# Performance work log

Measured on AMD Instinct MI355X. Metric: run time of the kernel, lower is better.

The kernel has to match this reference:

```python
import jax, jax.numpy as jnp
import numpy as np

NUM_LAYERS = 4
NUM_HEADS = 8
D_MODEL = 256
D_FF = 1024
UNC_THRESHOLD = 0.3
B, L = 2, 2048


def _layer_norm(x, g, b, eps=1e-5):
    m = jnp.mean(x, axis=-1, keepdims=True)
    v = jnp.mean((x - m) ** 2, axis=-1, keepdims=True)
    return (x - m) * jax.lax.rsqrt(v + eps) * g + b


def setup_inputs() -> dict:
    key = jax.random.key(0)
    ks = jax.random.split(key, 32)
    D, F, Ly = D_MODEL, D_FF, NUM_LAYERS
    w = lambda k, shape: jax.random.normal(k, shape, dtype=jnp.float32) * 0.02
    return {
        'x': jax.random.normal(ks[0], (B, L, D), dtype=jnp.float32),
        'Win': w(ks[1], (D, D)), 'bin_': jnp.zeros((D,), jnp.float32),
        'Wq': w(ks[2], (Ly, D, D)), 'bq': jnp.zeros((Ly, D), jnp.float32),
        'Wk': w(ks[3], (Ly, D, D)), 'bk': jnp.zeros((Ly, D), jnp.float32),
        'Wv': w(ks[4], (Ly, D, D)), 'bv': jnp.zeros((Ly, D), jnp.float32),
        'Wo': w(ks[5], (Ly, D, D)), 'bo': jnp.zeros((Ly, D), jnp.float32),
        'ev_scale': jnp.ones((Ly,), jnp.float32),
        'ev_bias': jnp.zeros((Ly,), jnp.float32),
        'W1': w(ks[6], (Ly, D, F)), 'b1': jnp.zeros((Ly, F), jnp.float32),
        'W2': w(ks[7], (Ly, F, D)), 'b2': jnp.zeros((Ly, D), jnp.float32),
        'n1g': jnp.ones((Ly, D), jnp.float32), 'n1b': jnp.zeros((Ly, D), jnp.float32),
        'n2g': jnp.ones((Ly, D), jnp.float32), 'n2b': jnp.zeros((Ly, D), jnp.float32),
        'fng': jnp.ones((D,), jnp.float32), 'fnb': jnp.zeros((D,), jnp.float32),
        'Wout': w(ks[8], (D, D)), 'bout': jnp.zeros((D,), jnp.float32),
    }


def _evidence_attention(x, Wq, bq, Wk, bk, Wv, bv, Wo, bo, scale, bias):
    b, l, d = x.shape
    hd = d // NUM_HEADS
    def heads(t):
        return t.reshape(b, l, NUM_HEADS, hd).transpose(0, 2, 1, 3)  # [B,H,L,hd]
    Q = heads(x @ Wq + bq)
    K = heads(x @ Wk + bk)
    V = heads(x @ Wv + bv)
    scores = jnp.einsum('bhqd,bhkd->bhqk', Q, K) / np.sqrt(hd).astype(np.float32)
    evidence = jnp.exp(scores) * scale + 1.0 + bias           # [B,H,L,L]
    denom = jnp.sum(evidence, axis=-1, keepdims=True)         # [B,H,L,1]
    uncertainty = (jnp.float32(l) / denom)[..., 0]            # [B,H,L]
    probs = evidence / denom
    attn = jnp.einsum('bhqk,bhkd->bhqd', probs, V)
    attn = attn.transpose(0, 2, 1, 3).reshape(b, l, d)
    return attn @ Wo + bo, uncertainty


def reference(x, Win, bin_, Wq, bq, Wk, bk, Wv, bv, Wo, bo, ev_scale, ev_bias,
              W1, b1, W2, b2, n1g, n1b, n2g, n2b, fng, fnb, Wout, bout):
    h = x @ Win + bin_
    total_unc = 0.0
    for i in range(NUM_LAYERS):
        attn_out, unc = _evidence_attention(
            _layer_norm(h, n1g[i], n1b[i]),
            Wq[i], bq[i], Wk[i], bk[i], Wv[i], bv[i], Wo[i], bo[i],
            ev_scale[i], ev_bias[i])
        h = h + attn_out
        ff = jax.nn.gelu(_layer_norm(h, n2g[i], n2b[i]) @ W1[i] + b1[i], approximate=False) @ W2[i] + b2[i]
        h = h + ff
        total_unc = total_unc + unc
    avg_unc = total_unc / NUM_LAYERS                          # [B,H,L]
    out = _layer_norm(h, fng, fnb) @ Wout + bout              # [B,L,D]
    should_abstain = avg_unc > UNC_THRESHOLD
    return out, avg_unc, should_abstain
```

## Files before the change

### kernel.cpp

```cpp
#include <hip/hip_runtime.h>
#include <hip/hip_bf16.h>
#include <math.h>

#define B_  2
#define L_  2048
#define D_  256
#define H_  8
#define HD_ 32
#define F_  1024
#define LY_ 4
#define M_  (B_*L_)

typedef __attribute__((ext_vector_type(8))) short bf16x8;
typedef __attribute__((ext_vector_type(4))) float f32x4;

static __device__ __forceinline__ short f2bf(float f) {
    return __builtin_bit_cast(short, __float2bfloat16(f));
}

static __device__ __forceinline__ void gload_lds16(const ushort* g, ushort* l) {
    __builtin_amdgcn_global_load_lds(
        (const __attribute__((address_space(1))) void*)g,
        (__attribute__((address_space(3))) void*)l, 16, 0, 0);
}

__global__ __launch_bounds__(256) void transpose_weights(
    const float* __restrict__ Win, const float* __restrict__ Wq,
    const float* __restrict__ Wk,  const float* __restrict__ Wv,
    const float* __restrict__ Wo,  const float* __restrict__ W1,
    const float* __restrict__ W2,  const float* __restrict__ Wout,
    ushort* __restrict__ T)
{
    const int bid = blockIdx.x;
    const float* src; ushort* dst; int K, N, tt;
    if (bid < 64)        { src = Win; dst = T; K = 256; N = 256; tt = bid; }
    else if (bid < 1088) {
        int i = bid - 64; int which = i >> 8; int l = (i >> 6) & 3; tt = i & 63;
        K = 256; N = 256;
        const float* s4[4] = {Wq, Wk, Wv, Wo};
        src = s4[which] + l * 65536;
        dst = T + 65536 * (1 + which * 4 + l);
    } else if (bid < 2112) {
        int i = bid - 1088; int l = i >> 8; tt = i & 255; K = 256; N = 1024;
        src = W1 + l * 262144; dst = T + 65536 * 17 + l * 262144;
    } else if (bid < 3136) {
        int i = bid - 2112; int l = i >> 8; tt = i & 255; K = 1024; N = 256;
        src = W2 + l * 262144; dst = T + 65536 * 17 + 1048576 + l * 262144;
    } else {
        src = Wout; dst = T + 65536 * 17 + 2097152; K = 256; N = 256; tt = bid - 3136;
    }
    const int ntn = N >> 5;
    const int tk = tt / ntn, tn = tt % ntn;
    __shared__ float ld[32][33];
    const int t = threadIdx.x;
    const int r = t >> 3, c4 = (t & 7) * 4;
    float4 v = *reinterpret_cast<const float4*>(&src[(size_t)(tk * 32 + r) * N + tn * 32 + c4]);
    ld[r][c4 + 0] = v.x; ld[r][c4 + 1] = v.y; ld[r][c4 + 2] = v.z; ld[r][c4 + 3] = v.w;
    __syncthreads();
    short4 o;
    o.x = f2bf(ld[c4 + 0][r]);
    o.y = f2bf(ld[c4 + 1][r]);
    o.z = f2bf(ld[c4 + 2][r]);
    o.w = f2bf(ld[c4 + 3][r]);
    *reinterpret_cast<short4*>(&dst[(size_t)(tn * 32 + r) * K + tk * 32 + c4]) = o;
}

template<int LNM>
__device__ __forceinline__ void core_f(
    const float* __restrict__ Hin, const float* __restrict__ lng,
    const float* __restrict__ lnb, const ushort* __restrict__ Wt,
    int row0, int col0, ushort* sLN, ushort* sW, f32x4 acc[2][2])
{
    const int tid  = threadIdx.x;
    const int lane = tid & 63;
    const int wid  = tid >> 6;
    const int wr = wid >> 1, wc = wid & 1;
    const int g = lane >> 4, nn = lane & 15;

    const int r0 = tid >> 3;
    const int sx = ((tid & 7) ^ (r0 & 7)) << 3;
    const ushort* Wp = &Wt[(size_t)(col0 + r0) * 256 + sx];
    ushort* ldsW = sW + wid * 512;
    gload_lds16(Wp,            ldsW);
    gload_lds16(Wp + 32 * 256, ldsW + 2048);

    const float4* hp = reinterpret_cast<const float4*>(Hin + (size_t)row0 * D_);
    float4 av[16];
#pragma unroll
    for (int j = 0; j < 16; ++j) av[j] = hp[j * 256 + tid];

    float4 g4, b4;
    if (LNM) {
        g4 = reinterpret_cast<const float4*>(lng)[lane];
        b4 = reinterpret_cast<const float4*>(lnb)[lane];
    }
#pragma unroll
    for (int j = 0; j < 16; ++j) {
        const float4 v = av[j];
        short4 o;
        if (LNM) {
            float s  = v.x + v.y + v.z + v.w;
            float s2 = v.x * v.x + v.y * v.y + v.z * v.z + v.w * v.w;
            s  += __shfl_xor(s, 1);  s  += __shfl_xor(s, 2);  s  += __shfl_xor(s, 4);
            s  += __shfl_xor(s, 8);  s  += __shfl_xor(s, 16); s  += __shfl_xor(s, 32);
            s2 += __shfl_xor(s2, 1); s2 += __shfl_xor(s2, 2); s2 += __shfl_xor(s2, 4);
            s2 += __shfl_xor(s2, 8); s2 += __shfl_xor(s2, 16); s2 += __shfl_xor(s2, 32);
            const float mean = s * (1.0f / D_);
            const float var  = s2 * (1.0f / D_) - mean * mean;
            const float rstd = rsqrtf(var + 1e-5f);
            o.x = f2bf((v.x - mean) * rstd * g4.x + b4.x);
            o.y = f2bf((v.y - mean) * rstd * g4.y + b4.y);
            o.z = f2bf((v.z - mean) * rstd * g4.z + b4.z);
            o.w = f2bf((v.w - mean) * rstd * g4.w + b4.w);
        } else {
            o.x = f2bf(v.x); o.y = f2bf(v.y); o.z = f2bf(v.z); o.w = f2bf(v.w);
        }
        *reinterpret_cast<short4*>(&sLN[(j * 4 + wid) * 264 + lane * 4]) = o;
    }
    __syncthreads();

    const int ra = (wr * 32 + nn) * 264, rb = ra + 16 * 264;
    const int rc = (wc * 32 + nn) * 64,  rd = rc + 16 * 64;
    const int m7 = nn & 7;

    int cur = 0;
#pragma unroll
    for (int k0 = 0; k0 < 256; k0 += 64) {
        if (k0 + 64 < 256) {
            ushort* lW = ldsW + (cur ^ 1) * 4096;
            gload_lds16(Wp + k0 + 64,            lW);
            gload_lds16(Wp + k0 + 64 + 32 * 256, lW + 2048);
        }
        const ushort* w = sW + cur * 4096;
#pragma unroll
        for (int sk = 0; sk < 2; ++sk) {
            const int ac = k0 + sk * 32 + g * 8;
            bf16x8 a0 = *reinterpret_cast<const bf16x8*>(&sLN[ra + ac]);
            bf16x8 a1 = *reinterpret_cast<const bf16x8*>(&sLN[rb + ac]);
            const int sw = ((sk * 4 + g) ^ m7) << 3;
            bf16x8 w0 = *reinterpret_cast<const bf16x8*>(&w[rc + sw]);
            bf16x8 w1 = *reinterpret_cast<const bf16x8*>(&w[rd + sw]);
            acc[0][0] = __builtin_amdgcn_mfma_f32_16x16x32_bf16(a0, w0, acc[0][0], 0, 0, 0);
            acc[0][1] = __builtin_amdgcn_mfma_f32_16x16x32_bf16(a0, w1, acc[0][1], 0, 0, 0);
            acc[1][0] = __builtin_amdgcn_mfma_f32_16x16x32_bf16(a1, w0, acc[1][0], 0, 0, 0);
            acc[1][1] = __builtin_amdgcn_mfma_f32_16x16x32_bf16(a1, w1, acc[1][1], 0, 0, 0);
        }
        __syncthreads();
        cur ^= 1;
    }
}

template<int LNM, int EPI, int OUTBF>
__global__ __launch_bounds__(256) void gemm_fused(
    const float* __restrict__ Hin, const float* __restrict__ lng,
    const float* __restrict__ lnb, const ushort* __restrict__ Wt,
    const float* __restrict__ bias, void* __restrict__ Cout, int N)
{
    __shared__ __align__(16) ushort sLN[64 * 264];
    __shared__ __align__(16) ushort sW[2 * 4096];
    const int row0 = blockIdx.y * 64, col0 = blockIdx.x * 64;
    f32x4 acc[2][2] = {};
    core_f<LNM>(Hin, lng, lnb, Wt, row0, col0, sLN, sW, acc);

    const int lane = threadIdx.x & 63;
    const int wid  = threadIdx.x >> 6;
    const int wr = wid >> 1, wc = wid & 1;
    const int g = lane >> 4, nn = lane & 15;
#pragma unroll
    for (int mi = 0; mi < 2; ++mi)
#pragma unroll
    for (int ni = 0; ni < 2; ++ni)
#pragma unroll
    for (int r = 0; r < 4; ++r) {
        const int m = row0 + wr * 32 + mi * 16 + g * 4 + r;
        const int c = col0 + wc * 32 + ni * 16 + nn;
        float v = acc[mi][ni][r] + bias[c];
        if (EPI == 1) v = 0.5f * v * (1.0f + erff(v * 0.70710678118654752f));
        if (OUTBF) ((ushort*)Cout)[(size_t)m * N + c] = (ushort)f2bf(v);
        else       ((float*)Cout)[(size_t)m * N + c] = v;
    }
}

__global__ __launch_bounds__(256) void gemm_qkv_f(
    const float* __restrict__ Hin, const float* __restrict__ lng,
    const float* __restrict__ lnb,
    const ushort* __restrict__ WqT, const ushort* __restrict__ WkT,
    const ushort* __restrict__ WvT,
    const float* __restrict__ bq, const float* __restrict__ bk,
    const float* __restrict__ bv,
    ushort* __restrict__ Qb, ushort* __restrict__ Kb, ushort* __restrict__ Vt)
{
    __shared__ __align__(16) ushort sLN[64 * 264];
    __shared__ __align__(16) ushort sW[2 * 4096];
    const int nb = blockIdx.x;
    const int wsel = nb >> 2;
    const int col0 = (nb & 3) * 64;
    const int row0 = blockIdx.y * 64;
    const ushort* Wt = (wsel == 0) ? WqT : (wsel == 1) ? WkT : WvT;
    const float* bias = (wsel == 0) ? bq : (wsel == 1) ? bk : bv;

    f32x4 acc[2][2] = {};
    core_f<1>(Hin, lng, lnb, Wt, row0, col0, sLN, sW, acc);

    const int lane = threadIdx.x & 63;
    const int wid  = threadIdx.x >> 6;
    const int wr = wid >> 1, wc = wid & 1;
    const int g = lane >> 4, nn = lane & 15;
    ushort* QK = (wsel == 0) ? Qb : Kb;
#pragma unroll
    for (int mi = 0; mi < 2; ++mi)
#pragma unroll
    for (int ni = 0; ni < 2; ++ni)
#pragma unroll
    for (int r = 0; r < 4; ++r) {
        const int m = row0 + wr * 32 + mi * 16 + g * 4 + r;
        const int c = col0 + wc * 32 + ni * 16 + nn;
        const float v = acc[mi][ni][r] + bias[c];
        if (wsel < 2) {
            QK[(size_t)m * D_ + c] = (ushort)f2bf(v);
        } else {
            const int b = m >> 11, l = m & 2047;
            const int h = c >> 5,  d = c & 31;
            Vt[(size_t)((b * 8 + h) * 32 + d) * L_ + l] = (ushort)f2bf(v);
        }
    }
}

__device__ __forceinline__ void gemm_core64(
    const ushort* __restrict__ A, const ushort* __restrict__ Wt, int K,
    int row0, int col0, ushort* sA, ushort* sW, f32x4 acc[2][2])
{
    const int tid  = threadIdx.x;
    const int lane = tid & 63;
    const int wid  = tid >> 6;
    const int wr = wid >> 1, wc = wid & 1;
    const int g = lane >> 4, nn = lane & 15;

    const int r0 = tid >> 3;
    const int sx = ((tid & 7) ^ (r0 & 7)) << 3;

    const ushort* Ap = &A[(size_t)(row0 + r0) * K + sx];
    const ushort* Wp = &Wt[(size_t)(col0 + r0) * K + sx];
    const size_t rstep = (size_t)32 * K;

    ushort* ldsA = sA + wid * 512;
    ushort* ldsW = sW + wid * 512;

    gload_lds16(Ap,         ldsA);
    gload_lds16(Ap + rstep, ldsA + 2048);
    gload_lds16(Wp,         ldsW);
    gload_lds16(Wp + rstep, ldsW + 2048);

    const int ra = (wr * 32 + nn) * 64, rb = ra + 16 * 64;
    const int rc = (wc * 32 + nn) * 64, rd = rc + 16 * 64;
    const int m7 = nn & 7;

    int cur = 0;
    __syncthreads();
    for (int k0 = 0; k0 < K; k0 += 64) {
        if (k0 + 64 < K) {
            ushort* lA = ldsA + (cur ^ 1) * 4096;
            ushort* lW = ldsW + (cur ^ 1) * 4096;
            gload_lds16(Ap + k0 + 64,         lA);
            gload_lds16(Ap + k0 + 64 + rstep, lA + 2048);
            gload_lds16(Wp + k0 + 64,         lW);
            gload_lds16(Wp + k0 + 64 + rstep, lW + 2048);
        }
        const ushort* a = sA + cur * 4096;
        const ushort* w = sW + cur * 4096;
#pragma unroll
        for (int sk = 0; sk < 2; ++sk) {
            const int sw = ((sk * 4 + g) ^ m7) << 3;
            bf16x8 a0 = *reinterpret_cast<const bf16x8*>(&a[ra + sw]);
            bf16x8 a1 = *reinterpret_cast<const bf16x8*>(&a[rb + sw]);
            bf16x8 w0 = *reinterpret_cast<const bf16x8*>(&w[rc + sw]);
            bf16x8 w1 = *reinterpret_cast<const bf16x8*>(&w[rd + sw]);
            acc[0][0] = __builtin_amdgcn_mfma_f32_16x16x32_bf16(a0, w0, acc[0][0], 0, 0, 0);
            acc[0][1] = __builtin_amdgcn_mfma_f32_16x16x32_bf16(a0, w1, acc[0][1], 0, 0, 0);
            acc[1][0] = __builtin_amdgcn_mfma_f32_16x16x32_bf16(a1, w0, acc[1][0], 0, 0, 0);
            acc[1][1] = __builtin_amdgcn_mfma_f32_16x16x32_bf16(a1, w1, acc[1][1], 0, 0, 0);
        }
        __syncthreads();
        cur ^= 1;
    }
}

__global__ __launch_bounds__(256) void gemm_res(
    const ushort* __restrict__ A, const ushort* __restrict__ Wt,
    const float* __restrict__ bias, float* __restrict__ C, int K)
{
    __shared__ __align__(16) ushort sA[2 * 4096];
    __shared__ __align__(16) ushort sW[2 * 4096];
    const int row0 = blockIdx.y * 64, col0 = blockIdx.x * 64;
    f32x4 acc[2][2] = {};
    gemm_core64(A, Wt, K, row0, col0, sA, sW, acc);

    const int lane = threadIdx.x & 63;
    const int wid  = threadIdx.x >> 6;
    const int wr = wid >> 1, wc = wid & 1;
    const int g = lane >> 4, nn = lane & 15;
#pragma unroll
    for (int mi = 0; mi < 2; ++mi)
#pragma unroll
    for (int ni = 0; ni < 2; ++ni)
#pragma unroll
    for (int r = 0; r < 4; ++r) {
        const int m = row0 + wr * 32 + mi * 16 + g * 4 + r;
        const int c = col0 + wc * 32 + ni * 16 + nn;
        C[(size_t)m * D_ + c] += acc[mi][ni][r] + bias[c];
    }
}

__global__ __launch_bounds__(256) void attn_mfma(
    const ushort* __restrict__ Qb, const ushort* __restrict__ Kb,
    const ushort* __restrict__ Vt, ushort* __restrict__ O,
    float* __restrict__ unc, const float* __restrict__ ev_scale,
    const float* __restrict__ ev_bias, int layer,
    float* __restrict__ out_unc, float* __restrict__ out_abst)
{
    const int bh = blockIdx.y;
    const int b  = bh >> 3;
    const int h  = bh & 7;
    const int tid  = threadIdx.x;
    const int wv   = tid >> 6;
    const int lane = tid & 63;
    const int g = lane >> 4;
    const int n = lane & 15;
    const int q  = blockIdx.x * 64 + wv * 16 + n;
    const float scale = ev_scale[layer];
    const float cb    = 1.0f + ev_bias[layer];
    const float isq   = 0.17677669529663687f;

    __shared__ __align__(16) ushort sK[2][64][40];
    __shared__ __align__(16) ushort sV[2][32][72];

    const size_t qk0 = (size_t)b * L_ * D_ + h * HD_;

    bf16x8 qf;
    {
        const bf16x8 qr = *reinterpret_cast<const bf16x8*>(&Qb[qk0 + (size_t)q * D_ + g * 8]);
#pragma unroll
        for (int j = 0; j < 8; ++j) {
            const float qv = __builtin_bit_cast(float, ((unsigned)(unsigned short)qr[j]) << 16);
            qf[j] = f2bf(qv * isq);
        }
    }
    bf16x8 ones;
#pragma unroll
    for (int j = 0; j < 8; ++j) ones[j] = (short)0x3F80;

    const int krow = tid >> 2, kch = (tid & 3) * 8;
    const int vrow = tid >> 3, vch = (tid & 7) * 8;
    const ushort* ksrc = Kb + qk0 + (size_t)krow * D_ + kch;
    const ushort* vsrc = Vt + (size_t)((b * 8 + h) * 32 + vrow) * L_ + vch;

    f32x4 acc0 = {0.f, 0.f, 0.f, 0.f};
    f32x4 acc1 = {0.f, 0.f, 0.f, 0.f};
    f32x4 accS = {0.f, 0.f, 0.f, 0.f};
    const f32x4 zero = {0.f, 0.f, 0.f, 0.f};

    bf16x8 kreg = *reinterpret_cast<const bf16x8*>(ksrc);
    bf16x8 vreg = *reinterpret_cast<const bf16x8*>(vsrc);

    int cur = 0;
    for (int t = 0; t < L_; t += 64) {
        *reinterpret_cast<bf16x8*>(&sK[cur][krow][kch]) = kreg;
        *reinterpret_cast<bf16x8*>(&sV[cur][vrow][vch]) = vreg;
        if (t + 64 < L_) {
            kreg = *reinterpret_cast<const bf16x8*>(ksrc + (size_t)(t + 64) * D_);
            vreg = *reinterpret_cast<const bf16x8*>(vsrc + (t + 64));
        }
        __syncthreads();

#pragma unroll
        for (int tt = 0; tt < 64; tt += 32) {
            bf16x8 kf0 = *reinterpret_cast<const bf16x8*>(&sK[cur][tt + n][g * 8]);
            bf16x8 kf1 = *reinterpret_cast<const bf16x8*>(&sK[cur][tt + 16 + n][g * 8]);

            f32x4 s0 = __builtin_amdgcn_mfma_f32_16x16x32_bf16(kf0, qf, zero, 0, 0, 0);
            f32x4 s1 = __builtin_amdgcn_mfma_f32_16x16x32_bf16(kf1, qf, zero, 0, 0, 0);

            short4 va = *reinterpret_cast<const short4*>(&sV[cur][n][tt + g * 4]);
            short4 vb = *reinterpret_cast<const short4*>(&sV[cur][n][tt + 16 + g * 4]);
            short4 vc = *reinterpret_cast<const short4*>(&sV[cur][n + 16][tt + g * 4]);
            short4 vd = *reinterpret_cast<const short4*>(&sV[cur][n + 16][tt + 16 + g * 4]);
            bf16x8 vf0 = {va.x, va.y, va.z, va.w, vb.x, vb.y, vb.z, vb.w};
            bf16x8 vf1 = {vc.x, vc.y, vc.z, vc.w, vd.x, vd.y, vd.z, vd.w};

            bf16x8 pa;
#pragma unroll
            for (int r = 0; r < 4; ++r) pa[r]     = f2bf(fmaf(__expf(s0[r]), scale, cb));
#pragma unroll
            for (int r = 0; r < 4; ++r) pa[r + 4] = f2bf(fmaf(__expf(s1[r]), scale, cb));

            acc0 = __builtin_amdgcn_mfma_f32_16x16x32_bf16(vf0, pa, acc0, 0, 0, 0);
            acc1 = __builtin_amdgcn_mfma_f32_16x16x32_bf16(vf1, pa, acc1, 0, 0, 0);
            accS = __builtin_amdgcn_mfma_f32_16x16x32_bf16(ones, pa, accS, 0, 0, 0);
        }
        cur ^= 1;
    }

    const float inv = 1.0f / accS[0];

    ushort* op = &O[qk0 + (size_t)q * D_ + g * 4];
    short4 o0 = {f2bf(acc0[0] * inv), f2bf(acc0[1] * inv), f2bf(acc0[2] * inv), f2bf(acc0[3] * inv)};
    short4 o1 = {f2bf(acc1[0] * inv), f2bf(acc1[1] * inv), f2bf(acc1[2] * inv), f2bf(acc1[3] * inv)};
    *reinterpret_cast<short4*>(op)      = o0;
    *reinterpret_cast<short4*>(op + 16) = o1;

    if (g == 0) {
        const float u = (float)L_ * inv;
        const int uidx = bh * L_ + q;
        if (layer == 0) {
            unc[uidx] = u;
        } else if (layer < LY_ - 1) {
            unc[uidx] += u;
        } else {
            const float avg = (unc[uidx] + u) * 0.25f;
            out_unc[uidx]  = avg;
            out_abst[uidx] = (avg > 0.3f) ? 1.0f : 0.0f;
        }
    }
}

extern "C" void kernel_launch(void* const* d_in, const int* in_sizes, int n_in,
                              void* d_out, int out_size, void* d_ws, size_t ws_size,
                              hipStream_t stream)
{
    const float* x    = (const float*)d_in[0];
    const float* Win  = (const float*)d_in[1];
    const float* bin_ = (const float*)d_in[2];
    const float* Wq   = (const float*)d_in[3];
    const float* bq   = (const float*)d_in[4];
    const float* Wk   = (const float*)d_in[5];
    const float* bk   = (const float*)d_in[6];
    const float* Wv   = (const float*)d_in[7];
    const float* bv   = (const float*)d_in[8];
    const float* Wo   = (const float*)d_in[9];
    const float* bo   = (const float*)d_in[10];
    const float* evs  = (const float*)d_in[11];
    const float* evb  = (const float*)d_in[12];
    const float* W1   = (const float*)d_in[13];
    const float* b1   = (const float*)d_in[14];
    const float* W2   = (const float*)d_in[15];
    const float* b2   = (const float*)d_in[16];
    const float* n1g  = (const float*)d_in[17];
    const float* n1b  = (const float*)d_in[18];
    const float* n2g  = (const float*)d_in[19];
    const float* n2b  = (const float*)d_in[20];
    const float* fng  = (const float*)d_in[21];
    const float* fnb  = (const float*)d_in[22];
    const float* Wout = (const float*)d_in[23];
    const float* bout = (const float*)d_in[24];

    char* ws = (char*)d_ws;
    float*  h    = (float*) (ws);
    ushort* Qb   = (ushort*)(ws + (6  << 20));
    ushort* Kb   = (ushort*)(ws + (8  << 20));
    ushort* Vt   = (ushort*)(ws + (10 << 20));
    ushort* Ob   = (ushort*)(ws + (12 << 20));
    ushort* ffb  = (ushort*)(ws + (4  << 20));
    float*  unc  = (float*) (ws + (14 << 20));
    ushort* T    = (ushort*)(ws + (15 << 20));

    ushort* winT  = T;
    ushort* woutT = T + 65536 * 17 + 2097152;

    float* out_main = (float*)d_out;
    float* out_unc  = out_main + M_ * D_;
    float* out_abst = out_unc + B_ * H_ * L_;

    const dim3 blk(256);
    const dim3 g256(4, 64);
    const dim3 g1024(16, 64);
    const dim3 gqkv(12, 64);
    const dim3 gattn(L_ / 64, B_ * H_);

    transpose_weights<<<3200, blk, 0, stream>>>(Win, Wq, Wk, Wv, Wo, W1, W2, Wout, T);
    gemm_fused<0, 0, 0><<<g256, blk, 0, stream>>>(x, nullptr, nullptr, winT, bin_, h, D_);

    for (int i = 0; i < LY_; ++i) {
        ushort* wqT = T + 65536 * (1 + i);
        ushort* wkT = T + 65536 * (5 + i);
        ushort* wvT = T + 65536 * (9 + i);
        ushort* woT = T + 65536 * (13 + i);
        ushort* w1T = T + 65536 * 17 + i * 262144;
        ushort* w2T = T + 65536 * 17 + 1048576 + i * 262144;

        gemm_qkv_f<<<gqkv, blk, 0, stream>>>(h, n1g + i * D_, n1b + i * D_,
                                             wqT, wkT, wvT,
                                             bq + i * D_, bk + i * D_, bv + i * D_,
                                             Qb, Kb, Vt);
        attn_mfma<<<gattn, blk, 0, stream>>>(Qb, Kb, Vt, Ob, unc, evs, evb, i,
                                             out_unc, out_abst);
        gemm_res<<<g256, blk, 0, stream>>>(Ob, woT, bo + i * D_, h, D_);
        gemm_fused<1, 1, 1><<<g1024, blk, 0, stream>>>(h, n2g + i * D_, n2b + i * D_,
                                                       w1T, b1 + i * F_, ffb, F_);
        gemm_res<<<g256, blk, 0, stream>>>(ffb, w2T, b2 + i * D_, h, F_);
    }

    gemm_fused<1, 0, 0><<<g256, blk, 0, stream>>>(h, fng, fnb, woutT, bout, out_main, D_);
}
```

Baseline: 323.2 us.

## Fuse out-proj, FFN and next-layer QKV into one row-block megakernel

Replaces the per-layer chain of separate GEMM launches (Wo residual, LN2+W1+GELU, W2 residual, LN1+QKV) with one kernel per layer. Each block handles 16 rows, keeps the residual and the FFN intermediate in LDS, and streams the full weight matrices through a double-buffered LDS tile. This removes the intermediate global round trips and several launches. In exchange, only 256 blocks run, each re-reads every weight matrix, and the large LDS footprint (about 120 KB) limits occupancy.

```diff
diff --git a/kernel.cpp b/kernel.cpp
--- a/kernel.cpp
+++ b/kernel.cpp
@@ -65,12 +65,13 @@
     *reinterpret_cast<short4*>(&dst[(size_t)(tn * 32 + r) * K + tk * 32 + c4]) = o;
 }
 
-template<int LNM>
-__device__ __forceinline__ void core_f(
-    const float* __restrict__ Hin, const float* __restrict__ lng,
-    const float* __restrict__ lnb, const ushort* __restrict__ Wt,
-    int row0, int col0, ushort* sLN, ushort* sW, f32x4 acc[2][2])
-{
+__global__ __launch_bounds__(256) void gemm_first(
+    const float* __restrict__ Hin, const ushort* __restrict__ Wt,
+    const float* __restrict__ bias, float* __restrict__ Cout)
+{
+    __shared__ __align__(16) ushort sLN[64 * 264];
+    __shared__ __align__(16) ushort sW[2 * 4096];
+    const int row0 = blockIdx.y * 64, col0 = blockIdx.x * 64;
     const int tid  = threadIdx.x;
     const int lane = tid & 63;
     const int wid  = tid >> 6;
@@ -85,36 +86,10 @@
     gload_lds16(Wp + 32 * 256, ldsW + 2048);
 
     const float4* hp = reinterpret_cast<const float4*>(Hin + (size_t)row0 * D_);
-    float4 av[16];
-#pragma unroll
-    for (int j = 0; j < 16; ++j) av[j] = hp[j * 256 + tid];
-
-    float4 g4, b4;
-    if (LNM) {
-        g4 = reinterpret_cast<const float4*>(lng)[lane];
-        b4 = reinterpret_cast<const float4*>(lnb)[lane];
-    }
 #pragma unroll
     for (int j = 0; j < 16; ++j) {
-        const float4 v = av[j];
-        short4 o;
-        if (LNM) {
-            float s  = v.x + v.y + v.z + v.w;
-            float s2 = v.x * v.x + v.y * v.y + v.z * v.z + v.w * v.w;
-            s  += __shfl_xor(s, 1);  s  += __shfl_xor(s, 2);  s  += __shfl_xor(s, 4);
-            s  += __shfl_xor(s, 8);  s  += __shfl_xor(s, 16); s  += __shfl_xor(s, 32);
-            s2 += __shfl_xor(s2, 1); s2 += __shfl_xor(s2, 2); s2 += __shfl_xor(s2, 4);
-            s2 += __shfl_xor(s2, 8); s2 += __shfl_xor(s2, 16); s2 += __shfl_xor(s2, 32);
-            const float mean = s * (1.0f / D_);
-            const float var  = s2 * (1.0f / D_) - mean * mean;
-            const float rstd = rsqrtf(var + 1e-5f);
-            o.x = f2bf((v.x - mean) * rstd * g4.x + b4.x);
-            o.y = f2bf((v.y - mean) * rstd * g4.y + b4.y);
-            o.z = f2bf((v.z - mean) * rstd * g4.z + b4.z);
-            o.w = f2bf((v.w - mean) * rstd * g4.w + b4.w);
-        } else {
-            o.x = f2bf(v.x); o.y = f2bf(v.y); o.z = f2bf(v.z); o.w = f2bf(v.w);
-        }
+        const float4 v = hp[j * 256 + tid];
+        short4 o = {f2bf(v.x), f2bf(v.y), f2bf(v.z), f2bf(v.w)};
         *reinterpret_cast<short4*>(&sLN[(j * 4 + wid) * 264 + lane * 4]) = o;
     }
     __syncthreads();
@@ -122,6 +97,7 @@
     const int ra = (wr * 32 + nn) * 264, rb = ra + 16 * 264;
     const int rc = (wc * 32 + nn) * 64,  rd = rc + 16 * 64;
     const int m7 = nn & 7;
+    f32x4 acc[2][2] = {};
 
     int cur = 0;
 #pragma unroll
@@ -148,24 +124,7 @@
         __syncthreads();
         cur ^= 1;
     }
-}
-
-template<int LNM, int EPI, int OUTBF>
-__global__ __launch_bounds__(256) void gemm_fused(
-    const float* __restrict__ Hin, const float* __restrict__ lng,
-    const float* __restrict__ lnb, const ushort* __restrict__ Wt,
-    const float* __restrict__ bias, void* __restrict__ Cout, int N)
-{
-    __shared__ __align__(16) ushort sLN[64 * 264];
-    __shared__ __align__(16) ushort sW[2 * 4096];
-    const int row0 = blockIdx.y * 64, col0 = blockIdx.x * 64;
-    f32x4 acc[2][2] = {};
-    core_f<LNM>(Hin, lng, lnb, Wt, row0, col0, sLN, sW, acc);
-
-    const int lane = threadIdx.x & 63;
-    const int wid  = threadIdx.x >> 6;
-    const int wr = wid >> 1, wc = wid & 1;
-    const int g = lane >> 4, nn = lane & 15;
+
 #pragma unroll
     for (int mi = 0; mi < 2; ++mi)
 #pragma unroll
@@ -174,140 +133,204 @@
     for (int r = 0; r < 4; ++r) {
         const int m = row0 + wr * 32 + mi * 16 + g * 4 + r;
         const int c = col0 + wc * 32 + ni * 16 + nn;
-        float v = acc[mi][ni][r] + bias[c];
-        if (EPI == 1) v = 0.5f * v * (1.0f + erff(v * 0.70710678118654752f));
-        if (OUTBF) ((ushort*)Cout)[(size_t)m * N + c] = (ushort)f2bf(v);
-        else       ((float*)Cout)[(size_t)m * N + c] = v;
-    }
-}
-
-__global__ __launch_bounds__(256) void gemm_qkv_f(
-    const float* __restrict__ Hin, const float* __restrict__ lng,
-    const float* __restrict__ lnb,
+        Cout[(size_t)m * D_ + c] = acc[mi][ni][r] + bias[c];
+    }
+}
+
+static __device__ __forceinline__ void stageW(
+    const ushort* __restrict__ W, int K, int k0, ushort* dst, int wid, int lane)
+{
+    const int rsub = lane >> 3;
+    const int slot = ((lane & 7) ^ (rsub & 7)) << 3;
+#pragma unroll
+    for (int q = 0; q < 8; ++q) {
+        const int r = (wid * 8 + q) * 8 + rsub;
+        gload_lds16(W + (size_t)r * K + k0 + slot, dst + (wid * 8 + q) * 512);
+    }
+}
+
+template<typename EPI>
+static __device__ __forceinline__ void gemm_nchunk(
+    const ushort* __restrict__ Wt, int K, const ushort* sA, int As,
+    ushort* sW, int wid, int lane, EPI epi)
+{
+    const int g = lane >> 4, nn = lane & 15;
+    stageW(Wt, K, 0, sW, wid, lane);
+    int cur = 0;
+    f32x4 acc[4] = {};
+    const int nkc = K >> 6;
+    for (int kc = 0; kc < nkc; ++kc) {
+        __syncthreads();
+        if (kc + 1 < nkc) stageW(Wt, K, (kc + 1) * 64, sW + (cur ^ 1) * 16384, wid, lane);
+        const ushort* w = sW + cur * 16384;
+#pragma unroll
+        for (int sk = 0; sk < 2; ++sk) {
+            bf16x8 a = *reinterpret_cast<const bf16x8*>(&sA[nn * As + kc * 64 + sk * 32 + g * 8]);
+            const int ws = ((sk * 4 + g) ^ (nn & 7)) << 3;
+#pragma unroll
+            for (int ni = 0; ni < 4; ++ni) {
+                const int wrow = wid * 64 + ni * 16 + nn;
+                bf16x8 wf = *reinterpret_cast<const bf16x8*>(&w[wrow * 64 + ws]);
+                acc[ni] = __builtin_amdgcn_mfma_f32_16x16x32_bf16(a, wf, acc[ni], 0, 0, 0);
+            }
+        }
+        cur ^= 1;
+    }
+    __syncthreads();
+    epi(acc);
+}
+
+static __device__ __forceinline__ void ln16(
+    const float* sH, ushort* sA, const float* __restrict__ gg,
+    const float* __restrict__ bb, int tid)
+{
+    const int row = tid >> 4, sc = (tid & 15) * 16;
+    float v[16];
+#pragma unroll
+    for (int j = 0; j < 16; ++j) v[j] = sH[row * 256 + sc + j];
+    float s = 0.f, s2 = 0.f;
+#pragma unroll
+    for (int j = 0; j < 16; ++j) { s += v[j]; s2 += v[j] * v[j]; }
+    s  += __shfl_xor(s, 1);  s  += __shfl_xor(s, 2);
+    s  += __shfl_xor(s, 4);  s  += __shfl_xor(s, 8);
+    s2 += __shfl_xor(s2, 1); s2 += __shfl_xor(s2, 2);
+    s2 += __shfl_xor(s2, 4); s2 += __shfl_xor(s2, 8);
+    const float mean = s * (1.0f / D_);
+    const float var  = s2 * (1.0f / D_) - mean * mean;
+    const float rstd = rsqrtf(var + 1e-5f);
+#pragma unroll
+    for (int j = 0; j < 16; ++j)
+        sA[row * 264 + sc + j] = (ushort)f2bf((v[j] - mean) * rstd * gg[sc + j] + bb[sc + j]);
+}
+
+template<int DO_FFN, int TAIL>
+__global__ __launch_bounds__(256) void mega(
+    const ushort* __restrict__ Ob, const ushort* __restrict__ WoT,
+    const float* __restrict__ bo, float* __restrict__ h,
+    const float* __restrict__ ln2g, const float* __restrict__ ln2b,
+    const ushort* __restrict__ W1T, const float* __restrict__ b1,
+    const ushort* __restrict__ W2T, const float* __restrict__ b2,
+    const float* __restrict__ ln1g, const float* __restrict__ ln1b,
     const ushort* __restrict__ WqT, const ushort* __restrict__ WkT,
     const ushort* __restrict__ WvT,
     const float* __restrict__ bq, const float* __restrict__ bk,
     const float* __restrict__ bv,
-    ushort* __restrict__ Qb, ushort* __restrict__ Kb, ushort* __restrict__ Vt)
-{
-    __shared__ __align__(16) ushort sLN[64 * 264];
-    __shared__ __align__(16) ushort sW[2 * 4096];
-    const int nb = blockIdx.x;
-    const int wsel = nb >> 2;
-    const int col0 = (nb & 3) * 64;
-    const int row0 = blockIdx.y * 64;
-    const ushort* Wt = (wsel == 0) ? WqT : (wsel == 1) ? WkT : WvT;
-    const float* bias = (wsel == 0) ? bq : (wsel == 1) ? bk : bv;
-
-    f32x4 acc[2][2] = {};
-    core_f<1>(Hin, lng, lnb, Wt, row0, col0, sLN, sW, acc);
-
-    const int lane = threadIdx.x & 63;
-    const int wid  = threadIdx.x >> 6;
-    const int wr = wid >> 1, wc = wid & 1;
-    const int g = lane >> 4, nn = lane & 15;
-    ushort* QK = (wsel == 0) ? Qb : Kb;
-#pragma unroll
-    for (int mi = 0; mi < 2; ++mi)
-#pragma unroll
-    for (int ni = 0; ni < 2; ++ni)
-#pragma unroll
-    for (int r = 0; r < 4; ++r) {
-        const int m = row0 + wr * 32 + mi * 16 + g * 4 + r;
-        const int c = col0 + wc * 32 + ni * 16 + nn;
-        const float v = acc[mi][ni][r] + bias[c];
-        if (wsel < 2) {
-            QK[(size_t)m * D_ + c] = (ushort)f2bf(v);
-        } else {
-            const int b = m >> 11, l = m & 2047;
-            const int h = c >> 5,  d = c & 31;
-            Vt[(size_t)((b * 8 + h) * 32 + d) * L_ + l] = (ushort)f2bf(v);
-        }
-    }
-}
-
-__device__ __forceinline__ void gemm_core64(
-    const ushort* __restrict__ A, const ushort* __restrict__ Wt, int K,
-    int row0, int col0, ushort* sA, ushort* sW, f32x4 acc[2][2])
-{
+    ushort* __restrict__ Qb, ushort* __restrict__ Kb, ushort* __restrict__ Vt,
+    float* __restrict__ outm)
+{
+    __shared__ __align__(16) ushort sW[2 * 16384];
+    __shared__ __align__(16) ushort sA[16 * 264];
+    __shared__ __align__(16) float  sH[16 * 256];
+    __shared__ __align__(16) ushort sF[16 * 1032];
+
     const int tid  = threadIdx.x;
     const int lane = tid & 63;
     const int wid  = tid >> 6;
-    const int wr = wid >> 1, wc = wid & 1;
     const int g = lane >> 4, nn = lane & 15;
-
-    const int r0 = tid >> 3;
-    const int sx = ((tid & 7) ^ (r0 & 7)) << 3;
-
-    const ushort* Ap = &A[(size_t)(row0 + r0) * K + sx];
-    const ushort* Wp = &Wt[(size_t)(col0 + r0) * K + sx];
-    const size_t rstep = (size_t)32 * K;
-
-    ushort* ldsA = sA + wid * 512;
-    ushort* ldsW = sW + wid * 512;
-
-    gload_lds16(Ap,         ldsA);
-    gload_lds16(Ap + rstep, ldsA + 2048);
-    gload_lds16(Wp,         ldsW);
-    gload_lds16(Wp + rstep, ldsW + 2048);
-
-    const int ra = (wr * 32 + nn) * 64, rb = ra + 16 * 64;
-    const int rc = (wc * 32 + nn) * 64, rd = rc + 16 * 64;
-    const int m7 = nn & 7;
-
-    int cur = 0;
+    const int row0 = blockIdx.x * 16;
+
+#pragma unroll
+    for (int q = 0; q < 4; ++q) {
+        float4 v = *reinterpret_cast<const float4*>(&h[(size_t)row0 * 256 + (q * 256 + tid) * 4]);
+        *reinterpret_cast<float4*>(&sH[(q * 256 + tid) * 4]) = v;
+    }
+
+    if constexpr (DO_FFN) {
+        {
+            const int r = tid >> 4, c = (tid & 15) * 16;
+            const ushort* s = Ob + (size_t)(row0 + r) * 256 + c;
+            *reinterpret_cast<bf16x8*>(&sA[r * 264 + c])     = *reinterpret_cast<const bf16x8*>(s);
+            *reinterpret_cast<bf16x8*>(&sA[r * 264 + c + 8]) = *reinterpret_cast<const bf16x8*>(s + 8);
+        }
+        gemm_nchunk(WoT, 256, sA, 264, sW, wid, lane, [&](const f32x4 (&acc)[4]) {
+#pragma unroll
+            for (int ni = 0; ni < 4; ++ni)
+#pragma unroll
+            for (int r = 0; r < 4; ++r) {
+                const int col = wid * 64 + ni * 16 + nn;
+                sH[(g * 4 + r) * 256 + col] += acc[ni][r] + bo[col];
+            }
+        });
+        __syncthreads();
+        ln16(sH, sA, ln2g, ln2b, tid);
+        __syncthreads();
+#pragma unroll
+        for (int nc = 0; nc < 4; ++nc) {
+            gemm_nchunk(W1T + (size_t)nc * 256 * 256, 256, sA, 264, sW, wid, lane,
+                        [&](const f32x4 (&acc)[4]) {
+#pragma unroll
+                for (int ni = 0; ni < 4; ++ni)
+#pragma unroll
+                for (int r = 0; r < 4; ++r) {
+                    const int col = nc * 256 + wid * 64 + ni * 16 + nn;
+                    float v = acc[ni][r] + b1[col];
+                    v = 0.5f * v * (1.0f + erff(v * 0.70710678118654752f));
+                    sF[(g * 4 + r) * 1032 + col] = (ushort)f2bf(v);
+                }
+            });
+        }
+        gemm_nchunk(W2T, 1024, sF, 1032, sW, wid, lane, [&](const f32x4 (&acc)[4]) {
+#pragma unroll
+            for (int ni = 0; ni < 4; ++ni)
+#pragma unroll
+            for (int r = 0; r < 4; ++r) {
+                const int col = wid * 64 + ni * 16 + nn;
+                sH[(g * 4 + r) * 256 + col] += acc[ni][r] + b2[col];
+            }
+        });
+        __syncthreads();
+#pragma unroll
+        for (int q = 0; q < 4; ++q) {
+            float4 v = *reinterpret_cast<const float4*>(&sH[(q * 256 + tid) * 4]);
+            *reinterpret_cast<float4*>(&h[(size_t)row0 * 256 + (q * 256 + tid) * 4]) = v;
+        }
+    }
+
     __syncthreads();
-    for (int k0 = 0; k0 < K; k0 += 64) {
-        if (k0 + 64 < K) {
-            ushort* lA = ldsA + (cur ^ 1) * 4096;
-            ushort* lW = ldsW + (cur ^ 1) * 4096;
-            gload_lds16(Ap + k0 + 64,         lA);
-            gload_lds16(Ap + k0 + 64 + rstep, lA + 2048);
-            gload_lds16(Wp + k0 + 64,         lW);
-            gload_lds16(Wp + k0 + 64 + rstep, lW + 2048);
-        }
-        const ushort* a = sA + cur * 4096;
-        const ushort* w = sW + cur * 4096;
-#pragma unroll
-        for (int sk = 0; sk < 2; ++sk) {
-            const int sw = ((sk * 4 + g) ^ m7) << 3;
-            bf16x8 a0 = *reinterpret_cast<const bf16x8*>(&a[ra + sw]);
-            bf16x8 a1 = *reinterpret_cast<const bf16x8*>(&a[rb + sw]);
-            bf16x8 w0 = *reinterpret_cast<const bf16x8*>(&w[rc + sw]);
-            bf16x8 w1 = *reinterpret_cast<const bf16x8*>(&w[rd + sw]);
-            acc[0][0] = __builtin_amdgcn_mfma_f32_16x16x32_bf16(a0, w0, acc[0][0], 0, 0, 0);
-            acc[0][1] = __builtin_amdgcn_mfma_f32_16x16x32_bf16(a0, w1, acc[0][1], 0, 0, 0);
-            acc[1][0] = __builtin_amdgcn_mfma_f32_16x16x32_bf16(a1, w0, acc[1][0], 0, 0, 0);
-            acc[1][1] = __builtin_amdgcn_mfma_f32_16x16x32_bf16(a1, w1, acc[1][1], 0, 0, 0);
-        }
-        __syncthreads();
-        cur ^= 1;
-    }
-}
-
-__global__ __launch_bounds__(256) void gemm_res(
-    const ushort* __restrict__ A, const ushort* __restrict__ Wt,
-    const float* __restrict__ bias, float* __restrict__ C, int K)
-{
-    __shared__ __align__(16) ushort sA[2 * 4096];
-    __shared__ __align__(16) ushort sW[2 * 4096];
-    const int row0 = blockIdx.y * 64, col0 = blockIdx.x * 64;
-    f32x4 acc[2][2] = {};
-    gemm_core64(A, Wt, K, row0, col0, sA, sW, acc);
-
-    const int lane = threadIdx.x & 63;
-    const int wid  = threadIdx.x >> 6;
-    const int wr = wid >> 1, wc = wid & 1;
-    const int g = lane >> 4, nn = lane & 15;
-#pragma unroll
-    for (int mi = 0; mi < 2; ++mi)
-#pragma unroll
-    for (int ni = 0; ni < 2; ++ni)
-#pragma unroll
-    for (int r = 0; r < 4; ++r) {
-        const int m = row0 + wr * 32 + mi * 16 + g * 4 + r;
-        const int c = col0 + wc * 32 + ni * 16 + nn;
-        C[(size_t)m * D_ + c] += acc[mi][ni][r] + bias[c];
+    ln16(sH, sA, ln1g, ln1b, tid);
+    __syncthreads();
+
+    if constexpr (TAIL == 0) {
+        gemm_nchunk(WqT, 256, sA, 264, sW, wid, lane, [&](const f32x4 (&acc)[4]) {
+#pragma unroll
+            for (int ni = 0; ni < 4; ++ni)
+#pragma unroll
+            for (int r = 0; r < 4; ++r) {
+                const int col = wid * 64 + ni * 16 + nn;
+                Qb[(size_t)(row0 + g * 4 + r) * 256 + col] = (ushort)f2bf(acc[ni][r] + bq[col]);
+            }
+        });
+        gemm_nchunk(WkT, 256, sA, 264, sW, wid, lane, [&](const f32x4 (&acc)[4]) {
+#pragma unroll
+            for (int ni = 0; ni < 4; ++ni)
+#pragma unroll
+            for (int r = 0; r < 4; ++r) {
+                const int col = wid * 64 + ni * 16 + nn;
+                Kb[(size_t)(row0 + g * 4 + r) * 256 + col] = (ushort)f2bf(acc[ni][r] + bk[col]);
+            }
+        });
+        gemm_nchunk(WvT, 256, sA, 264, sW, wid, lane, [&](const f32x4 (&acc)[4]) {
+#pragma unroll
+            for (int ni = 0; ni < 4; ++ni)
+#pragma unroll
+            for (int r = 0; r < 4; ++r) {
+                const int m = row0 + g * 4 + r;
+                const int col = wid * 64 + ni * 16 + nn;
+                const int b = m >> 11, l = m & 2047;
+                const int hh = col >> 5, d = col & 31;
+                Vt[(size_t)((b * 8 + hh) * 32 + d) * L_ + l] = (ushort)f2bf(acc[ni][r] + bv[col]);
+            }
+        });
+    } else {
+        gemm_nchunk(WqT, 256, sA, 264, sW, wid, lane, [&](const f32x4 (&acc)[4]) {
+#pragma unroll
+            for (int ni = 0; ni < 4; ++ni)
+#pragma unroll
+            for (int r = 0; r < 4; ++r) {
+                const int col = wid * 64 + ni * 16 + nn;
+                outm[(size_t)(row0 + g * 4 + r) * 256 + col] = acc[ni][r] + bq[col];
+            }
+        });
     }
 }
 
@@ -459,7 +482,6 @@
     ushort* Kb   = (ushort*)(ws + (8  << 20));
     ushort* Vt   = (ushort*)(ws + (10 << 20));
     ushort* Ob   = (ushort*)(ws + (12 << 20));
-    ushort* ffb  = (ushort*)(ws + (4  << 20));
     float*  unc  = (float*) (ws + (14 << 20));
     ushort* T    = (ushort*)(ws + (15 << 20));
 
@@ -471,33 +493,43 @@
     float* out_abst = out_unc + B_ * H_ * L_;
 
     const dim3 blk(256);
-    const dim3 g256(4, 64);
-    const dim3 g1024(16, 64);
-    const dim3 gqkv(12, 64);
+    const dim3 gfirst(4, 64);
     const dim3 gattn(L_ / 64, B_ * H_);
 
     transpose_weights<<<3200, blk, 0, stream>>>(Win, Wq, Wk, Wv, Wo, W1, W2, Wout, T);
-    gemm_fused<0, 0, 0><<<g256, blk, 0, stream>>>(x, nullptr, nullptr, winT, bin_, h, D_);
+    gemm_first<<<gfirst, blk, 0, stream>>>(x, winT, bin_, h);
+
+    mega<0, 0><<<256, blk, 0, stream>>>(nullptr, nullptr, nullptr, h,
+                                        nullptr, nullptr, nullptr, nullptr,
+                                        nullptr, nullptr,
+                                        n1g, n1b,
+                                        T + 65536 * 1, T + 65536 * 5, T + 65536 * 9,
+                                        bq, bk, bv, Qb, Kb, Vt, nullptr);
 
     for (int i = 0; i < LY_; ++i) {
-        ushort* wqT = T + 65536 * (1 + i);
-        ushort* wkT = T + 65536 * (5 + i);
-        ushort* wvT = T + 65536 * (9 + i);
         ushort* woT = T + 65536 * (13 + i);
         ushort* w1T = T + 65536 * 17 + i * 262144;
         ushort* w2T = T + 65536 * 17 + 1048576 + i * 262144;
 
-        gemm_qkv_f<<<gqkv, blk, 0, stream>>>(h, n1g + i * D_, n1b + i * D_,
-                                             wqT, wkT, wvT,
-                                             bq + i * D_, bk + i * D_, bv + i * D_,
-                                             Qb, Kb, Vt);
         attn_mfma<<<gattn, blk, 0, stream>>>(Qb, Kb, Vt, Ob, unc, evs, evb, i,
                                              out_unc, out_abst);
-        gemm_res<<<g256, blk, 0, stream>>>(Ob, woT, bo + i * D_, h, D_);
-        gemm_fused<1, 1, 1><<<g1024, blk, 0, stream>>>(h, n2g + i * D_, n2b + i * D_,
-                                                       w1T, b1 + i * F_, ffb, F_);
-        gemm_res<<<g256, blk, 0, stream>>>(ffb, w2T, b2 + i * D_, h, F_);
-    }
-
-    gemm_fused<1, 0, 0><<<g256, blk, 0, stream>>>(h, fng, fnb, woutT, bout, out_main, D_);
-}
+        if (i < LY_ - 1) {
+            const int j = i + 1;
+            mega<1, 0><<<256, blk, 0, stream>>>(
+                Ob, woT, bo + i * D_, h, n2g + i * D_, n2b + i * D_,
+                w1T, b1 + i * F_, w2T, b2 + i * D_,
+                n1g + j * D_, n1b + j * D_,
+                T + 65536 * (1 + j), T + 65536 * (5 + j), T + 65536 * (9 + j),
+                bq + j * D_, bk + j * D_, bv + j * D_,
+                Qb, Kb, Vt, nullptr);
+        } else {
+            mega<1, 1><<<256, blk, 0, stream>>>(
+                Ob, woT, bo + i * D_, h, n2g + i * D_, n2b + i * D_,
+                w1T, b1 + i * F_, w2T, b2 + i * D_,
+                fng, fnb,
+                woutT, nullptr, nullptr,
+                bout, nullptr, nullptr,
+                nullptr, nullptr, nullptr, out_main);
+        }
+    }
+}
```

After: 316.1 us. 1.02x faster.
